# Kernel tuning notes

Hardware: AMD Instinct MI355X
Metric: run time of the kernel (lower is better)

Reference implementation:

```python
import jax, jax.numpy as jnp
import numpy as np

N_NODES = 100000
N_EDGES = 1600000
D_IN = 128
D_HID = 128
D_OUT = 64


def spmm(vals, row, col, x):
    # sparse [N,N] @ dense [N,D]: out[r] = sum_e vals[e] * x[col[e]] for row[e]==r
    msgs = vals[:, None] * x[col]            # [E, D]
    return jax.ops.segment_sum(msgs, row, num_segments=N_NODES)


def setup_inputs() -> dict:
    key = jax.random.key(0)
    ks = jax.random.split(key, 8)
    x = jax.random.normal(ks[0], (N_NODES, D_IN), dtype=jnp.float32)
    vals = jax.random.uniform(ks[1], (N_EDGES,), dtype=jnp.float32)
    W1 = jax.random.normal(ks[2], (D_IN, D_HID), dtype=jnp.float32) * (1.0 / np.sqrt(D_IN))
    b1 = jnp.zeros((D_HID,), dtype=jnp.float32)
    W2 = jax.random.normal(ks[3], (D_HID, D_HID), dtype=jnp.float32) * (1.0 / np.sqrt(D_HID))
    b2 = jnp.zeros((D_HID,), dtype=jnp.float32)
    W3 = jax.random.normal(ks[4], (D_HID, D_OUT), dtype=jnp.float32) * (1.0 / np.sqrt(D_HID))
    b3 = jnp.zeros((D_OUT,), dtype=jnp.float32)
    row = jax.random.randint(ks[5], (N_EDGES,), 0, N_NODES, dtype=jnp.int32)
    col = jax.random.randint(ks[6], (N_EDGES,), 0, N_NODES, dtype=jnp.int32)
    return {"x": x, "vals": vals, "W1": W1, "b1": b1, "W2": W2, "b2": b2,
            "W3": W3, "b3": b3, "row": row, "col": col}


def reference(x, vals, W1, b1, W2, b2, W3, b3, row, col):
    # GCNConv 1: linear -> spmm -> relu
    h = jax.nn.relu(spmm(vals, row, col, x @ W1 + b1))
    # GCNConv 2: linear -> spmm -> relu
    h = jax.nn.relu(spmm(vals, row, col, h @ W2 + b2))
    # GCNConv 3 (output): linear -> spmm, no activation
    out = spmm(vals, row, col, h @ W3 + b3)
    return out
```

## Files before the change

kernel.cpp:

```cpp
#include <hip/hip_runtime.h>

#define N_NODES 100000
#define N_EDGES 1600000

#define NBK 782
#define EPB 8192
#define NBA 196
#define CAPE 4096

typedef __attribute__((ext_vector_type(8))) short short8;
typedef __attribute__((ext_vector_type(4))) float f32x4;

__device__ __forceinline__ ushort f2bf(float f) {
    uint u = __float_as_uint(f);
    return (ushort)((u + 0x7fff + ((u >> 16) & 1)) >> 16);
}
__device__ __forceinline__ float bflo(uint p) { return __uint_as_float(p << 16); }
__device__ __forceinline__ float bfhi(uint p) { return __uint_as_float(p & 0xffff0000u); }


__global__ void __launch_bounds__(1024) binA_k(const int* __restrict__ row,
                                               const int* __restrict__ col,
                                               const float* __restrict__ vals,
                                               int2* __restrict__ tmp,
                                               int* __restrict__ gcount,
                                               int* __restrict__ offT) {
    __shared__ int h[NBK];
    __shared__ int cur[NBK];
    __shared__ int wpart[16];
    int t = threadIdx.x;
    int lane = t & 63;
    int base = blockIdx.x * EPB;

    int rr[8], cc[8];
    float vv[8];
#pragma unroll
    for (int u = 0; u < 8; ++u) {
        int e = base + u * 1024 + t;
        bool ok = (e < N_EDGES);
        rr[u] = ok ? row[e] : -1;
        cc[u] = ok ? col[e] : 0;
        vv[u] = ok ? vals[e] : 0.f;
    }

    if (t < NBK) h[t] = 0;
    __syncthreads();
#pragma unroll
    for (int u = 0; u < 8; ++u)
        if (rr[u] >= 0) atomicAdd(&h[rr[u] >> 7], 1);
    __syncthreads();
    int hv = (t < NBK) ? h[t] : 0;
    if (hv) atomicAdd(&gcount[t], hv);

    int v = hv;
    for (int off = 1; off < 64; off <<= 1) {
        int u2 = __shfl_up(v, off);
        if (lane >= off) v += u2;
    }
    if (lane == 63) wpart[t >> 6] = v;
    __syncthreads();
    if (t == 0) {
        int acc = 0;
#pragma unroll
        for (int i = 0; i < 16; ++i) { int w = wpart[i]; wpart[i] = acc; acc += w; }
    }
    __syncthreads();
    v += wpart[t >> 6];
    if (t < NBK) {
        int ex = v - hv;
        cur[t] = ex;
        offT[t * NBA + blockIdx.x] = ex;
    }
    if (t == NBK - 1) offT[NBK * NBA + blockIdx.x] = v;
    __syncthreads();
#pragma unroll
    for (int u = 0; u < 8; ++u) {
        if (rr[u] >= 0) {
            int p = atomicAdd(&cur[rr[u] >> 7], 1);
            int2 w;
            w.x = ((rr[u] & 127) << 17) | cc[u];
            w.y = __float_as_int(vv[u]);
            tmp[base + p] = w;
        }
    }
}

__global__ void __launch_bounds__(1024) bscan_k(const int* __restrict__ gcount,
                                                int* __restrict__ bstart,
                                                int* __restrict__ rowptr) {
    __shared__ int wpart[16];
    int t = threadIdx.x;
    int lane = t & 63;
    int g = (t < NBK) ? gcount[t] : 0;
    int v = g;
    for (int off = 1; off < 64; off <<= 1) {
        int u = __shfl_up(v, off);
        if (lane >= off) v += u;
    }
    if (lane == 63) wpart[t >> 6] = v;
    __syncthreads();
    if (t == 0) {
        int acc = 0;
#pragma unroll
        for (int i = 0; i < 16; ++i) { int w = wpart[i]; wpart[i] = acc; acc += w; }
    }
    __syncthreads();
    v += wpart[t >> 6];
    if (t < NBK) bstart[t] = v - g;
    if (t == 0) rowptr[N_NODES] = N_EDGES;
}


__global__ void __launch_bounds__(256) binB_k(const int2* __restrict__ tmp,
                                              const int* __restrict__ offT,
                                              const int* __restrict__ bstart,
                                              int* __restrict__ rowptr,
                                              int2* __restrict__ ep) {
    __shared__ int goff[NBA];
    __shared__ int scnt[NBA];
    __shared__ int sdst[NBA];
    __shared__ int h[128];
    __shared__ int cur[128];
    __shared__ int2 ebuf[CAPE];
    __shared__ int wpart[4];
    __shared__ int hp;
    int b = blockIdx.x, t = threadIdx.x;
    int lane = t & 63;

    int c = 0;
    if (t < NBA) {
        int o0 = offT[b * NBA + t];
        int o1 = offT[(b + 1) * NBA + t];
        c = o1 - o0;
        goff[t] = t * EPB + o0;
        scnt[t] = c;
    }
    int v = c;
    for (int off = 1; off < 64; off <<= 1) {
        int u = __shfl_up(v, off);
        if (lane >= off) v += u;
    }
    if (lane == 63) wpart[t >> 6] = v;
    if (t < 128) h[t] = 0;
    __syncthreads();
    if (t == 0) {
        int acc = 0;
#pragma unroll
        for (int i = 0; i < 4; ++i) { int w = wpart[i]; wpart[i] = acc; acc += w; }
    }
    __syncthreads();
    v += wpart[t >> 6];
    if (t < NBA) sdst[t] = v - c;
    __syncthreads();

    int grp = t >> 4, gl = t & 15;
    for (int s = grp; s < NBA; s += 16) {
        int n = scnt[s], go = goff[s], dd = sdst[s];
        for (int i = gl; i < n; i += 16) {
            int2 e = tmp[go + i];
            atomicAdd(&h[e.x >> 17], 1);
            ebuf[dd + i] = e;
        }
    }
    __syncthreads();
    int hv = (t < 128) ? h[t] : 0;
    int sv = hv;
    for (int off = 1; off < 64; off <<= 1) {
        int u = __shfl_up(sv, off);
        if (lane >= off) sv += u;
    }
    if (t == 63) hp = sv;
    __syncthreads();
    int bs = bstart[b];
    if (t < 128) {
        int inc = sv + ((t >= 64) ? hp : 0);
        int ex = inc - hv;
        cur[t] = ex;
        int r = (b << 7) + t;
        if (r < N_NODES) rowptr[r] = bs + ex;
    }
    __syncthreads();
    int T = sdst[NBA - 1] + scnt[NBA - 1];
    for (int j = t; j < T; j += 256) {
        int2 e = ebuf[j];
        int p = atomicAdd(&cur[e.x >> 17], 1);
        int2 w;
        w.x = e.x & 0x1ffff;
        w.y = e.y;
        ep[bs + p] = w;
    }
}


__global__ void wcvt_k(const float* __restrict__ W1, const float* __restrict__ W2,
                       const float* __restrict__ W3, ushort* __restrict__ Wt1,
                       ushort* __restrict__ Wt2, ushort* __restrict__ Wt3,
                       int* __restrict__ gcount) {
    int i = blockIdx.x * 256 + threadIdx.x;
    if (i < NBK) gcount[i] = 0;
    if (i < 16384) {
        int n = i >> 7, k = i & 127;
        Wt1[i] = f2bf(W1[k * 128 + n]);
        Wt2[i] = f2bf(W2[k * 128 + n]);
    }
    if (i < 8192) {
        int n = i >> 7, k = i & 127;
        Wt3[i] = f2bf(W3[k * 64 + n]);
    }
}


template <int DN, bool AF32>
__global__ void __launch_bounds__(256) gemm_k(const void* __restrict__ Xa,
                                              const ushort* __restrict__ Wt,
                                              const float* __restrict__ bias,
                                              ushort* __restrict__ Y) {
    constexpr int NT = DN / 16;
    const ushort* Xb = (const ushort*)Xa;
    const float* Xf = (const float*)Xa;
    int wv = threadIdx.x >> 6;
    int l = threadIdx.x & 63;
    int lg = l >> 4, lm = l & 15;
    int rbase = blockIdx.x * 64 + wv * 16;

    int arow = rbase + lm;
    if (arow > N_NODES - 1) arow = N_NODES - 1;

    f32x4 acc[NT];
#pragma unroll
    for (int n = 0; n < NT; n++) acc[n] = (f32x4){0.f, 0.f, 0.f, 0.f};

#pragma unroll
    for (int kk = 0; kk < 4; ++kk) {
        short8 a;
        if constexpr (AF32) {
            const float* ap = Xf + (size_t)arow * 128 + kk * 32 + lg * 8;
            float4 u = *(const float4*)ap;
            float4 v = *(const float4*)(ap + 4);
            a = (short8){(short)f2bf(u.x), (short)f2bf(u.y), (short)f2bf(u.z), (short)f2bf(u.w),
                         (short)f2bf(v.x), (short)f2bf(v.y), (short)f2bf(v.z), (short)f2bf(v.w)};
        } else {
            a = *(const short8*)(Xb + (size_t)arow * 128 + kk * 32 + lg * 8);
        }
#pragma unroll
        for (int n = 0; n < NT; ++n) {
            short8 b = *(const short8*)(Wt + (size_t)(n * 16 + lm) * 128 + kk * 32 + lg * 8);
            acc[n] = __builtin_amdgcn_mfma_f32_16x16x32_bf16(a, b, acc[n], 0, 0, 0);
        }
    }

    int r0 = rbase + lg * 4;
#pragma unroll
    for (int n = 0; n < NT; ++n) {
        int c = n * 16 + lm;
        float bj = bias[c];
#pragma unroll
        for (int i = 0; i < 4; ++i) {
            int r = r0 + i;
            if (r < N_NODES) Y[(size_t)r * DN + c] = f2bf(acc[n][i] + bj);
        }
    }
}


#define SPMM_BODY(EPREAD)                                                     \
    if (D == 128) {                                                           \
        const uint4* xp = (const uint4*)xb;                                   \
        float a0 = 0.f, a1 = 0.f, a2 = 0.f, a3 = 0.f;                         \
        float a4 = 0.f, a5 = 0.f, a6 = 0.f, a7 = 0.f;                         \
        int i = s;                                                            \
        for (; i + 4 <= e; i += 4) {                                          \
            int2 e0 = EPREAD(i), e1 = EPREAD(i + 1);                          \
            int2 e2 = EPREAD(i + 2), e3 = EPREAD(i + 3);                      \
            uint4 x0 = xp[e0.x * 16 + hl];                                    \
            uint4 x1 = xp[e1.x * 16 + hl];                                    \
            uint4 x2 = xp[e2.x * 16 + hl];                                    \
            uint4 x3 = xp[e3.x * 16 + hl];                                    \
            float v0 = __int_as_float(e0.y), v1 = __int_as_float(e1.y);       \
            float v2 = __int_as_float(e2.y), v3 = __int_as_float(e3.y);       \
            a0 = fmaf(v0, bflo(x0.x), a0); a1 = fmaf(v0, bfhi(x0.x), a1);     \
            a2 = fmaf(v0, bflo(x0.y), a2); a3 = fmaf(v0, bfhi(x0.y), a3);     \
            a4 = fmaf(v0, bflo(x0.z), a4); a5 = fmaf(v0, bfhi(x0.z), a5);     \
            a6 = fmaf(v0, bflo(x0.w), a6); a7 = fmaf(v0, bfhi(x0.w), a7);     \
            a0 = fmaf(v1, bflo(x1.x), a0); a1 = fmaf(v1, bfhi(x1.x), a1);     \
            a2 = fmaf(v1, bflo(x1.y), a2); a3 = fmaf(v1, bfhi(x1.y), a3);     \
            a4 = fmaf(v1, bflo(x1.z), a4); a5 = fmaf(v1, bfhi(x1.z), a5);     \
            a6 = fmaf(v1, bflo(x1.w), a6); a7 = fmaf(v1, bfhi(x1.w), a7);     \
            a0 = fmaf(v2, bflo(x2.x), a0); a1 = fmaf(v2, bfhi(x2.x), a1);     \
            a2 = fmaf(v2, bflo(x2.y), a2); a3 = fmaf(v2, bfhi(x2.y), a3);     \
            a4 = fmaf(v2, bflo(x2.z), a4); a5 = fmaf(v2, bfhi(x2.z), a5);     \
            a6 = fmaf(v2, bflo(x2.w), a6); a7 = fmaf(v2, bfhi(x2.w), a7);     \
            a0 = fmaf(v3, bflo(x3.x), a0); a1 = fmaf(v3, bfhi(x3.x), a1);     \
            a2 = fmaf(v3, bflo(x3.y), a2); a3 = fmaf(v3, bfhi(x3.y), a3);     \
            a4 = fmaf(v3, bflo(x3.z), a4); a5 = fmaf(v3, bfhi(x3.z), a5);     \
            a6 = fmaf(v3, bflo(x3.w), a6); a7 = fmaf(v3, bfhi(x3.w), a7);     \
        }                                                                     \
        for (; i < e; ++i) {                                                  \
            int2 e0 = EPREAD(i);                                              \
            uint4 x0 = xp[e0.x * 16 + hl];                                    \
            float v0 = __int_as_float(e0.y);                                  \
            a0 = fmaf(v0, bflo(x0.x), a0); a1 = fmaf(v0, bfhi(x0.x), a1);     \
            a2 = fmaf(v0, bflo(x0.y), a2); a3 = fmaf(v0, bfhi(x0.y), a3);     \
            a4 = fmaf(v0, bflo(x0.z), a4); a5 = fmaf(v0, bfhi(x0.z), a5);     \
            a6 = fmaf(v0, bflo(x0.w), a6); a7 = fmaf(v0, bfhi(x0.w), a7);     \
        }                                                                     \
        if (RELU) {                                                           \
            a0 = fmaxf(a0, 0.f); a1 = fmaxf(a1, 0.f);                         \
            a2 = fmaxf(a2, 0.f); a3 = fmaxf(a3, 0.f);                         \
            a4 = fmaxf(a4, 0.f); a5 = fmaxf(a5, 0.f);                         \
            a6 = fmaxf(a6, 0.f); a7 = fmaxf(a7, 0.f);                         \
        }                                                                     \
        uint4 o;                                                              \
        o.x = (uint)f2bf(a0) | ((uint)f2bf(a1) << 16);                        \
        o.y = (uint)f2bf(a2) | ((uint)f2bf(a3) << 16);                        \
        o.z = (uint)f2bf(a4) | ((uint)f2bf(a5) << 16);                        \
        o.w = (uint)f2bf(a6) | ((uint)f2bf(a7) << 16);                        \
        ((uint4*)y)[w * 16 + hl] = o;                                         \
    } else {                                                                  \
        const uint2* xp = (const uint2*)xb;                                   \
        float a0 = 0.f, a1 = 0.f, a2 = 0.f, a3 = 0.f;                         \
        int i = s;                                                            \
        for (; i + 4 <= e; i += 4) {                                          \
            int2 e0 = EPREAD(i), e1 = EPREAD(i + 1);                          \
            int2 e2 = EPREAD(i + 2), e3 = EPREAD(i + 3);                      \
            uint2 x0 = xp[e0.x * 16 + hl];                                    \
            uint2 x1 = xp[e1.x * 16 + hl];                                    \
            uint2 x2 = xp[e2.x * 16 + hl];                                    \
            uint2 x3 = xp[e3.x * 16 + hl];                                    \
            float v0 = __int_as_float(e0.y), v1 = __int_as_float(e1.y);       \
            float v2 = __int_as_float(e2.y), v3 = __int_as_float(e3.y);       \
            a0 = fmaf(v0, bflo(x0.x), a0); a1 = fmaf(v0, bfhi(x0.x), a1);     \
            a2 = fmaf(v0, bflo(x0.y), a2); a3 = fmaf(v0, bfhi(x0.y), a3);     \
            a0 = fmaf(v1, bflo(x1.x), a0); a1 = fmaf(v1, bfhi(x1.x), a1);     \
            a2 = fmaf(v1, bflo(x1.y), a2); a3 = fmaf(v1, bfhi(x1.y), a3);     \
            a0 = fmaf(v2, bflo(x2.x), a0); a1 = fmaf(v2, bfhi(x2.x), a1);     \
            a2 = fmaf(v2, bflo(x2.y), a2); a3 = fmaf(v2, bfhi(x2.y), a3);     \
            a0 = fmaf(v3, bflo(x3.x), a0); a1 = fmaf(v3, bfhi(x3.x), a1);     \
            a2 = fmaf(v3, bflo(x3.y), a2); a3 = fmaf(v3, bfhi(x3.y), a3);     \
        }                                                                     \
        for (; i < e; ++i) {                                                  \
            int2 e0 = EPREAD(i);                                              \
            uint2 x0 = xp[e0.x * 16 + hl];                                    \
            float v0 = __int_as_float(e0.y);                                  \
            a0 = fmaf(v0, bflo(x0.x), a0); a1 = fmaf(v0, bfhi(x0.x), a1);     \
            a2 = fmaf(v0, bflo(x0.y), a2); a3 = fmaf(v0, bfhi(x0.y), a3);     \
        }                                                                     \
        if (RELU) {                                                           \
            a0 = fmaxf(a0, 0.f); a1 = fmaxf(a1, 0.f);                         \
            a2 = fmaxf(a2, 0.f); a3 = fmaxf(a3, 0.f);                         \
        }                                                                     \
        float4 o; o.x = a0; o.y = a1; o.z = a2; o.w = a3;                     \
        ((float4*)y)[w * 16 + hl] = o;                                        \
    }

template <int D, bool RELU>
__global__ void __launch_bounds__(256) spmm_k(const int* __restrict__ rowptr,
                                              const int2* __restrict__ ep,
                                              const ushort* __restrict__ xb,
                                              void* __restrict__ y) {
    constexpr int CAP = 1536;
    __shared__ int2 eb[CAP];
    __shared__ int sh_s0, sh_n;
    int t = threadIdx.x;
    int g = t >> 4, hl = t & 15;
    int rbase = blockIdx.x * 16;
    int w = rbase + g;

    if (t == 0) {
        int s0 = rowptr[rbase];
        int rend = rbase + 16; if (rend > N_NODES) rend = N_NODES;
        sh_s0 = s0;
        sh_n = rowptr[rend] - s0;
    }
    __syncthreads();
    int s0 = sh_s0, n = sh_n;
    bool inlds = (n <= CAP);
    if (inlds) {
        for (int j = t; j < n; j += 256) eb[j] = ep[s0 + j];
    }
    __syncthreads();
    if (w >= N_NODES) return;
    int s = rowptr[w], e = rowptr[w + 1];

    if (inlds) {
        s -= s0; e -= s0;
#define EPL(i) eb[i]
        SPMM_BODY(EPL)
#undef EPL
    } else {
#define EPG(i) ep[i]
        SPMM_BODY(EPG)
#undef EPG
    }
}


extern "C" void kernel_launch(void* const* d_in, const int* in_sizes, int n_in,
                              void* d_out, int out_size, void* d_ws, size_t ws_size,
                              hipStream_t stream) {
    const float* x    = (const float*)d_in[0];
    const float* vals = (const float*)d_in[1];
    const float* W1   = (const float*)d_in[2];
    const float* b1   = (const float*)d_in[3];
    const float* W2   = (const float*)d_in[4];
    const float* b2   = (const float*)d_in[5];
    const float* W3   = (const float*)d_in[6];
    const float* b3   = (const float*)d_in[7];
    const int* row    = (const int*)d_in[8];
    const int* col    = (const int*)d_in[9];
    float* out = (float*)d_out;

    char* ws = (char*)d_ws;
    int2*   ep     = (int2*)  (ws + 0);
    int*    rowptr = (int*)   (ws + 12800000);
    int*    gcount = (int*)   (ws + 13250000);
    int*    bstart = (int*)   (ws + 13260000);
    ushort* Wt1    = (ushort*)(ws + 13601024);
    ushort* Wt2    = (ushort*)(ws + 13633792);
    ushort* Wt3    = (ushort*)(ws + 13666560);
    int*    offT   = (int*)   (ws + 13700096);
    ushort* g64    = (ushort*)(ws + 16000000);
    ushort* g      = (ushort*)(ws + 41600000);
    ushort* sbuf   = (ushort*)(ws + 67200000);

    int2* tmp = (int2*)g;

    hipLaunchKernelGGL(wcvt_k, dim3(64), dim3(256), 0, stream,
                       W1, W2, W3, Wt1, Wt2, Wt3, gcount);

    hipLaunchKernelGGL(binA_k, dim3(NBA), dim3(1024), 0, stream,
                       row, col, vals, tmp, gcount, offT);
    hipLaunchKernelGGL(bscan_k, dim3(1), dim3(1024), 0, stream, gcount, bstart, rowptr);
    hipLaunchKernelGGL(binB_k, dim3(NBK), dim3(256), 0, stream,
                       tmp, offT, bstart, rowptr, ep);

    const int GEMM_GRID = (N_NODES + 63) / 64;
    const int SPMM_GRID = (N_NODES + 15) / 16;

    hipLaunchKernelGGL((gemm_k<128, true>), dim3(GEMM_GRID), dim3(256), 0, stream, x, Wt1, b1, g);
    hipLaunchKernelGGL((spmm_k<128, true>), dim3(SPMM_GRID), dim3(256), 0, stream,
                       rowptr, ep, g, sbuf);
    hipLaunchKernelGGL((gemm_k<128, false>), dim3(GEMM_GRID), dim3(256), 0, stream, sbuf, Wt2, b2, g);
    hipLaunchKernelGGL((spmm_k<128, true>), dim3(SPMM_GRID), dim3(256), 0, stream,
                       rowptr, ep, g, sbuf);
    hipLaunchKernelGGL((gemm_k<64, false>), dim3(GEMM_GRID), dim3(256), 0, stream, sbuf, Wt3, b3, g64);
    hipLaunchKernelGGL((spmm_k<64, false>), dim3(SPMM_GRID), dim3(256), 0, stream,
                       rowptr, ep, g64, out);
}
```

Before: 293.9 us.

## Fuse edge binning with first GEMM and fold bucket scan into binB

The first-layer GEMM blocks run inside the same launch as the edge binning pass, so the dense x@W1 work overlaps the scatter-bound binning. The scratch buffer moves from g to sbuf so the two no longer collide. The separate single-block scan kernel is removed: each binB block sums the preceding bucket counts itself. That saves two launches but adds redundant prefix summation of up to 782 values per block. The GEMM blocks now use 1024 threads, 16 waves of 16 rows each.

```diff
diff --git a/kernel.cpp b/kernel.cpp
--- a/kernel.cpp
+++ b/kernel.cpp
@@ -19,18 +19,16 @@
 __device__ __forceinline__ float bfhi(uint p) { return __uint_as_float(p & 0xffff0000u); }
 
 
-__global__ void __launch_bounds__(1024) binA_k(const int* __restrict__ row,
-                                               const int* __restrict__ col,
-                                               const float* __restrict__ vals,
-                                               int2* __restrict__ tmp,
-                                               int* __restrict__ gcount,
-                                               int* __restrict__ offT) {
+__device__ void binA_body(int bid, const int* __restrict__ row,
+                          const int* __restrict__ col, const float* __restrict__ vals,
+                          int2* __restrict__ tmp, int* __restrict__ gcount,
+                          int* __restrict__ offT) {
     __shared__ int h[NBK];
     __shared__ int cur[NBK];
     __shared__ int wpart[16];
     int t = threadIdx.x;
     int lane = t & 63;
-    int base = blockIdx.x * EPB;
+    int base = bid * EPB;
 
     int rr[8], cc[8];
     float vv[8];
@@ -69,9 +67,9 @@
     if (t < NBK) {
         int ex = v - hv;
         cur[t] = ex;
-        offT[t * NBA + blockIdx.x] = ex;
-    }
-    if (t == NBK - 1) offT[NBK * NBA + blockIdx.x] = v;
+        offT[t * NBA + bid] = ex;
+    }
+    if (t == NBK - 1) offT[NBK * NBA + bid] = v;
     __syncthreads();
 #pragma unroll
     for (int u = 0; u < 8; ++u) {
@@ -85,35 +83,70 @@
     }
 }
 
-__global__ void __launch_bounds__(1024) bscan_k(const int* __restrict__ gcount,
-                                                int* __restrict__ bstart,
-                                                int* __restrict__ rowptr) {
-    __shared__ int wpart[16];
-    int t = threadIdx.x;
-    int lane = t & 63;
-    int g = (t < NBK) ? gcount[t] : 0;
-    int v = g;
-    for (int off = 1; off < 64; off <<= 1) {
-        int u = __shfl_up(v, off);
-        if (lane >= off) v += u;
-    }
-    if (lane == 63) wpart[t >> 6] = v;
-    __syncthreads();
-    if (t == 0) {
-        int acc = 0;
-#pragma unroll
-        for (int i = 0; i < 16; ++i) { int w = wpart[i]; wpart[i] = acc; acc += w; }
-    }
-    __syncthreads();
-    v += wpart[t >> 6];
-    if (t < NBK) bstart[t] = v - g;
-    if (t == 0) rowptr[N_NODES] = N_EDGES;
+
+__device__ void gemmA_body(int bid, const float* __restrict__ Xf,
+                           const ushort* __restrict__ Wt,
+                           const float* __restrict__ bias, ushort* __restrict__ Y) {
+    int wv = threadIdx.x >> 6;
+    int l = threadIdx.x & 63;
+    int lg = l >> 4, lm = l & 15;
+    int rbase = bid * 256 + wv * 16;
+
+    int arow = rbase + lm;
+    if (arow > N_NODES - 1) arow = N_NODES - 1;
+
+    f32x4 acc[8];
+#pragma unroll
+    for (int n = 0; n < 8; n++) acc[n] = (f32x4){0.f, 0.f, 0.f, 0.f};
+
+#pragma unroll
+    for (int kk = 0; kk < 4; ++kk) {
+        const float* ap = Xf + (size_t)arow * 128 + kk * 32 + lg * 8;
+        float4 u = *(const float4*)ap;
+        float4 v = *(const float4*)(ap + 4);
+        short8 a = (short8){(short)f2bf(u.x), (short)f2bf(u.y), (short)f2bf(u.z),
+                            (short)f2bf(u.w), (short)f2bf(v.x), (short)f2bf(v.y),
+                            (short)f2bf(v.z), (short)f2bf(v.w)};
+#pragma unroll
+        for (int n = 0; n < 8; ++n) {
+            short8 b = *(const short8*)(Wt + (size_t)(n * 16 + lm) * 128 + kk * 32 + lg * 8);
+            acc[n] = __builtin_amdgcn_mfma_f32_16x16x32_bf16(a, b, acc[n], 0, 0, 0);
+        }
+    }
+
+    int r0 = rbase + lg * 4;
+#pragma unroll
+    for (int n = 0; n < 8; ++n) {
+        int c = n * 16 + lm;
+        float bj = bias[c];
+#pragma unroll
+        for (int i = 0; i < 4; ++i) {
+            int r = r0 + i;
+            if (r < N_NODES) Y[(size_t)r * 128 + c] = f2bf(acc[n][i] + bj);
+        }
+    }
+}
+
+__global__ void __launch_bounds__(1024) fusedA_k(const int* __restrict__ row,
+                                                 const int* __restrict__ col,
+                                                 const float* __restrict__ vals,
+                                                 int2* __restrict__ tmp,
+                                                 int* __restrict__ gcount,
+                                                 int* __restrict__ offT,
+                                                 const float* __restrict__ x,
+                                                 const ushort* __restrict__ Wt1,
+                                                 const float* __restrict__ b1,
+                                                 ushort* __restrict__ g) {
+    if (blockIdx.x < NBA)
+        binA_body(blockIdx.x, row, col, vals, tmp, gcount, offT);
+    else
+        gemmA_body(blockIdx.x - NBA, x, Wt1, b1, g);
 }
 
 
 __global__ void __launch_bounds__(256) binB_k(const int2* __restrict__ tmp,
                                               const int* __restrict__ offT,
-                                              const int* __restrict__ bstart,
+                                              const int* __restrict__ gcount,
                                               int* __restrict__ rowptr,
                                               int2* __restrict__ ep) {
     __shared__ int goff[NBA];
@@ -123,9 +156,17 @@
     __shared__ int cur[128];
     __shared__ int2 ebuf[CAPE];
     __shared__ int wpart[4];
+    __shared__ int wq[4];
     __shared__ int hp;
     int b = blockIdx.x, t = threadIdx.x;
     int lane = t & 63;
+
+    int part = 0;
+    for (int i = t; i < b; i += 256) part += gcount[i];
+#pragma unroll
+    for (int off = 1; off < 64; off <<= 1) part += __shfl_xor(part, off);
+    if (lane == 0) wq[t >> 6] = part;
+    if (b == 0 && t == 0) rowptr[N_NODES] = N_EDGES;
 
     int c = 0;
     if (t < NBA) {
@@ -171,7 +212,7 @@
     }
     if (t == 63) hp = sv;
     __syncthreads();
-    int bs = bstart[b];
+    int bs = wq[0] + wq[1] + wq[2] + wq[3];
     if (t < 128) {
         int inc = sv + ((t >= 64) ? hp : 0);
         int ex = inc - hv;
@@ -210,14 +251,12 @@
 }
 
 
-template <int DN, bool AF32>
-__global__ void __launch_bounds__(256) gemm_k(const void* __restrict__ Xa,
+template <int DN>
+__global__ void __launch_bounds__(256) gemm_k(const ushort* __restrict__ Xb,
                                               const ushort* __restrict__ Wt,
                                               const float* __restrict__ bias,
                                               ushort* __restrict__ Y) {
     constexpr int NT = DN / 16;
-    const ushort* Xb = (const ushort*)Xa;
-    const float* Xf = (const float*)Xa;
     int wv = threadIdx.x >> 6;
     int l = threadIdx.x & 63;
     int lg = l >> 4, lm = l & 15;
@@ -232,16 +271,7 @@
 
 #pragma unroll
     for (int kk = 0; kk < 4; ++kk) {
-        short8 a;
-        if constexpr (AF32) {
-            const float* ap = Xf + (size_t)arow * 128 + kk * 32 + lg * 8;
-            float4 u = *(const float4*)ap;
-            float4 v = *(const float4*)(ap + 4);
-            a = (short8){(short)f2bf(u.x), (short)f2bf(u.y), (short)f2bf(u.z), (short)f2bf(u.w),
-                         (short)f2bf(v.x), (short)f2bf(v.y), (short)f2bf(v.z), (short)f2bf(v.w)};
-        } else {
-            a = *(const short8*)(Xb + (size_t)arow * 128 + kk * 32 + lg * 8);
-        }
+        short8 a = *(const short8*)(Xb + (size_t)arow * 128 + kk * 32 + lg * 8);
 #pragma unroll
         for (int n = 0; n < NT; ++n) {
             short8 b = *(const short8*)(Wt + (size_t)(n * 16 + lm) * 128 + kk * 32 + lg * 8);
@@ -414,7 +444,6 @@
     int2*   ep     = (int2*)  (ws + 0);
     int*    rowptr = (int*)   (ws + 12800000);
     int*    gcount = (int*)   (ws + 13250000);
-    int*    bstart = (int*)   (ws + 13260000);
     ushort* Wt1    = (ushort*)(ws + 13601024);
     ushort* Wt2    = (ushort*)(ws + 13633792);
     ushort* Wt3    = (ushort*)(ws + 13666560);
@@ -423,27 +452,27 @@
     ushort* g      = (ushort*)(ws + 41600000);
     ushort* sbuf   = (ushort*)(ws + 67200000);
 
-    int2* tmp = (int2*)g;
+    int2* tmp = (int2*)sbuf;
 
     hipLaunchKernelGGL(wcvt_k, dim3(64), dim3(256), 0, stream,
                        W1, W2, W3, Wt1, Wt2, Wt3, gcount);
 
-    hipLaunchKernelGGL(binA_k, dim3(NBA), dim3(1024), 0, stream,
-                       row, col, vals, tmp, gcount, offT);
-    hipLaunchKernelGGL(bscan_k, dim3(1), dim3(1024), 0, stream, gcount, bstart, rowptr);
+    const int GEMM1_BLKS = (N_NODES + 255) / 256;
+    hipLaunchKernelGGL(fusedA_k, dim3(NBA + GEMM1_BLKS), dim3(1024), 0, stream,
+                       row, col, vals, tmp, gcount, offT, x, Wt1, b1, g);
+
     hipLaunchKernelGGL(binB_k, dim3(NBK), dim3(256), 0, stream,
-                       tmp, offT, bstart, rowptr, ep);
+                       tmp, offT, gcount, rowptr, ep);
 
     const int GEMM_GRID = (N_NODES + 63) / 64;
     const int SPMM_GRID = (N_NODES + 15) / 16;
 
-    hipLaunchKernelGGL((gemm_k<128, true>), dim3(GEMM_GRID), dim3(256), 0, stream, x, Wt1, b1, g);
     hipLaunchKernelGGL((spmm_k<128, true>), dim3(SPMM_GRID), dim3(256), 0, stream,
                        rowptr, ep, g, sbuf);
-    hipLaunchKernelGGL((gemm_k<128, false>), dim3(GEMM_GRID), dim3(256), 0, stream, sbuf, Wt2, b2, g);
+    hipLaunchKernelGGL((gemm_k<128>), dim3(GEMM_GRID), dim3(256), 0, stream, sbuf, Wt2, b2, g);
     hipLaunchKernelGGL((spmm_k<128, true>), dim3(SPMM_GRID), dim3(256), 0, stream,
                        rowptr, ep, g, sbuf);
-    hipLaunchKernelGGL((gemm_k<64, false>), dim3(GEMM_GRID), dim3(256), 0, stream, sbuf, Wt3, b3, g64);
+    hipLaunchKernelGGL((gemm_k<64>), dim3(GEMM_GRID), dim3(256), 0, stream, sbuf, Wt3, b3, g64);
     hipLaunchKernelGGL((spmm_k<64, false>), dim3(SPMM_GRID), dim3(256), 0, stream,
                        rowptr, ep, g64, out);
 }
```

New measurement: 296.0 us. About the same (+0.7%).
